# Optimization experiments

Hardware: AMD Instinct MI355X
Metric: run time of the kernel (lower is better)

Reference implementation:

```python
import jax, jax.numpy as jnp
import numpy as np

NB_HEAD = 16
SIZE_PER_HEAD = 64
D_MODEL = NB_HEAD * SIZE_PER_HEAD  # 1024
B, S = 4, 2048
NEG_BIG = 1e10


def setup_inputs() -> dict:
    key = jax.random.key(0)
    ks = jax.random.split(key, 9)
    glorot = lambda k, shape: jax.random.uniform(
        k, shape, jnp.float32, -1.0, 1.0) * np.sqrt(6.0 / (shape[0] + shape[1]))
    return {
        "Q_emb": jax.random.normal(ks[0], (B, S, D_MODEL), jnp.float32),
        "K_emb": jax.random.normal(ks[1], (B, S, D_MODEL), jnp.float32),
        "V_emb": jax.random.normal(ks[2], (B, S, D_MODEL), jnp.float32),
        "Q_ini": jax.random.randint(ks[3], (B, S), 0, 50),
        "K_ini": jax.random.randint(ks[4], (B, S), 0, 50),
        "WQ": glorot(ks[5], (D_MODEL, D_MODEL)),
        "WK": glorot(ks[6], (D_MODEL, D_MODEL)),
        "WV": glorot(ks[7], (D_MODEL, D_MODEL)),
        "WO": glorot(ks[8], (D_MODEL, D_MODEL)),
    }


def _proj(x, W):
    # [B,S,D] @ [D, H*dh] -> [B,H,S,dh]
    b, s, _ = x.shape
    y = jnp.einsum('bsd,de->bse', x, W)
    return y.reshape(b, s, NB_HEAD, SIZE_PER_HEAD).transpose(0, 2, 1, 3)


def reference(Q_emb, K_emb, V_emb, Q_ini, K_ini, WQ, WK, WV, WO):
    b, sq, _ = Q_emb.shape
    sk = K_emb.shape[1]
    q = _proj(Q_emb, WQ)
    k = _proj(K_emb, WK)
    v = _proj(V_emb, WV)
    scores = jnp.einsum('bhqd,bhkd->bhqk', q, k) / jnp.sqrt(
        jnp.asarray(SIZE_PER_HEAD, scores_dtype := q.dtype))
    # pad mask: 1 where key token id != 0, broadcast over queries
    pad = (K_ini != 0).astype(scores.dtype)[:, None, None, :]  # [B,1,1,Sk]
    # sub mask: cumsum of eye along rows == lower-triangular causal mask
    causal = jnp.tril(jnp.ones((sq, sk), scores.dtype))[None, None]  # [1,1,Sq,Sk]
    mask = jnp.minimum(pad, causal)
    scores = scores - (1.0 - mask) * NEG_BIG
    attn = jax.nn.softmax(scores, axis=-1)
    ctx = jnp.einsum('bhqk,bhkd->bhqd', attn, v)
    ctx = ctx.transpose(0, 2, 1, 3).reshape(b, sq, NB_HEAD * SIZE_PER_HEAD)
    return jnp.einsum('bsd,de->bse', ctx, WO)
```

## Files before the change

kernel.cpp:

```cpp
#include <hip/hip_runtime.h>

typedef __bf16 bf16_t;
typedef __bf16 bf16x8 __attribute__((ext_vector_type(8)));
typedef __bf16 bf16x4 __attribute__((ext_vector_type(4)));
typedef float  f32x4  __attribute__((ext_vector_type(4)));

#define S_LEN 2048
#define NH    16
#define DH    64
#define DM    1024
#define BATCH 4

static __device__ __forceinline__ f32x4 mfma16(bf16x8 a, bf16x8 b, f32x4 c) {
    return __builtin_amdgcn_mfma_f32_16x16x32_bf16(a, b, c, 0, 0, 0);
}

static __device__ __forceinline__ f32x4 fmax4(f32x4 a, f32x4 b) {
    f32x4 r;
    r[0] = fmaxf(a[0], b[0]); r[1] = fmaxf(a[1], b[1]);
    r[2] = fmaxf(a[2], b[2]); r[3] = fmaxf(a[3], b[3]);
    return r;
}

static __device__ __forceinline__ void gl_lds16(const bf16_t* g, bf16_t* l) {
    __builtin_amdgcn_global_load_lds(
        (const __attribute__((address_space(1))) unsigned int*)g,
        (__attribute__((address_space(3))) unsigned int*)l, 16, 0, 0);
}

__global__ __launch_bounds__(256) void cvt_bf16(const float* __restrict__ s,
                                                bf16_t* __restrict__ d, int n) {
    int i = (blockIdx.x * 256 + threadIdx.x) * 8;
    if (i >= n) return;
    const float4* q = (const float4*)(s + i);
    float4 a = q[0], b = q[1];
    bf16x8 r;
    r[0] = (bf16_t)a.x; r[1] = (bf16_t)a.y; r[2] = (bf16_t)a.z; r[3] = (bf16_t)a.w;
    r[4] = (bf16_t)b.x; r[5] = (bf16_t)b.y; r[6] = (bf16_t)b.z; r[7] = (bf16_t)b.w;
    *(bf16x8*)(d + i) = r;
}

__global__ __launch_bounds__(256) void wtrans(const float* __restrict__ W,
                                              bf16_t* __restrict__ Wt, float scale) {
    __shared__ bf16_t tile[32][33];
    int x = threadIdx.x, ty = threadIdx.y;
    int bx = blockIdx.x * 32, by = blockIdx.y * 32;
#pragma unroll
    for (int i = 0; i < 4; ++i) {
        int y = ty * 4 + i;
        tile[y][x] = (bf16_t)(W[(by + y) * DM + bx + x] * scale);
    }
    __syncthreads();
#pragma unroll
    for (int i = 0; i < 4; ++i) {
        int y = ty * 4 + i;
        Wt[(bx + y) * DM + by + x] = tile[x][y];
    }
}

__global__ __launch_bounds__(256) void btrans(const bf16_t* __restrict__ src,
                                              bf16_t* __restrict__ dst,
                                              int R, int C) {
    __shared__ bf16_t tile[32][33];
    int x = threadIdx.x, ty = threadIdx.y;
    int bx = blockIdx.x * 32, by = blockIdx.y * 32;
#pragma unroll
    for (int i = 0; i < 4; ++i) {
        int y = ty * 4 + i;
        tile[y][x] = src[(size_t)(by + y) * C + bx + x];
    }
    __syncthreads();
#pragma unroll
    for (int i = 0; i < 4; ++i) {
        int y = ty * 4 + i;
        dst[(size_t)(bx + y) * R + by + x] = tile[x][y];
    }
}

template <typename CT>
__global__ __launch_bounds__(256) void gemm_nt_128(const bf16_t* __restrict__ A,
                                                   const bf16_t* __restrict__ Bt,
                                                   CT* __restrict__ C,
                                                   int M, int N, int K, float alpha) {
    __shared__ __align__(16) bf16_t As[128 * 32];
    __shared__ __align__(16) bf16_t Bs[128 * 32];
    int tid = threadIdx.x, wave = tid >> 6, lane = tid & 63;
    int l15 = lane & 15, quad = lane >> 4;
    int wm = wave >> 1, wn = wave & 1;
    int bm = blockIdx.x * 128, bn = blockIdx.y * 128;
    int lrow = lane >> 2, lk = (lane & 3) << 3;

    f32x4 acc[4][4] = {};

    for (int k0 = 0; k0 < K; k0 += 32) {
#pragma unroll
        for (int c = 0; c < 2; ++c) {
            int r = wave * 32 + c * 16 + lrow;
            gl_lds16(A  + (size_t)(bm + r) * K + k0 + lk, As + (wave * 2 + c) * 512);
            gl_lds16(Bt + (size_t)(bn + r) * K + k0 + lk, Bs + (wave * 2 + c) * 512);
        }
        __syncthreads();

        bf16x8 af[4], bfr[4];
#pragma unroll
        for (int i = 0; i < 4; ++i)
            af[i] = *(const bf16x8*)(As + (wm * 64 + i * 16 + l15) * 32 + quad * 8);
#pragma unroll
        for (int j = 0; j < 4; ++j)
            bfr[j] = *(const bf16x8*)(Bs + (wn * 64 + j * 16 + l15) * 32 + quad * 8);
#pragma unroll
        for (int i = 0; i < 4; ++i)
#pragma unroll
            for (int j = 0; j < 4; ++j)
                acc[i][j] = mfma16(af[i], bfr[j], acc[i][j]);
        __syncthreads();
    }

#pragma unroll
    for (int i = 0; i < 4; ++i)
#pragma unroll
        for (int r = 0; r < 4; ++r) {
            int row = bm + wm * 64 + i * 16 + quad * 4 + r;
#pragma unroll
            for (int j = 0; j < 4; ++j)
                C[(size_t)row * N + bn + wn * 64 + j * 16 + l15] =
                    (CT)(acc[i][j][r] * alpha);
        }
}

__global__ __launch_bounds__(256) void vmean_kernel(const bf16_t* __restrict__ Vp,
                                                    float* __restrict__ Vm) {
    __shared__ float red[4][64];
    int z = blockIdx.y;
    int c = blockIdx.x * 64 + (threadIdx.x & 63);
    int rg = threadIdx.x >> 6;
    const bf16_t* p = Vp + (size_t)z * S_LEN * DM + (size_t)rg * (S_LEN / 4) * DM + c;
    float s = 0.f;
    for (int r = 0; r < S_LEN / 4; ++r) s += (float)p[(size_t)r * DM];
    red[rg][threadIdx.x & 63] = s;
    __syncthreads();
    if (threadIdx.x < 64) {
        float t = red[0][threadIdx.x] + red[1][threadIdx.x] +
                  red[2][threadIdx.x] + red[3][threadIdx.x];
        Vm[z * DM + blockIdx.x * 64 + threadIdx.x] = t * (1.0f / S_LEN);
    }
}

__global__ __launch_bounds__(256) void attn_kernel(const bf16_t* __restrict__ Qp,
                                                   const bf16_t* __restrict__ Kp,
                                                   const bf16_t* __restrict__ VT,
                                                   const int* __restrict__ Kini,
                                                   const float* __restrict__ Vmean,
                                                   bf16_t* __restrict__ ctx,
                                                   int ldv, int nqt) {
    __shared__ __align__(16) bf16_t Ks[64 * 72];
    __shared__ __align__(16) bf16_t VsT[64 * 72];
    __shared__ __align__(16) bf16_t Ps[4][16 * 72];
    __shared__ bf16_t padb[2048];

    int bid = blockIdx.x;
    int qt = nqt - 1 - (bid >> 6);
    int hz = bid & 63;
    int h = hz & 15, z = hz >> 4;
    int tid = threadIdx.x, wave = tid >> 6, lane = tid & 63;
    int l15 = lane & 15, quad = lane >> 4;
    int qbase = qt * 64 + wave * 16;
    size_t rowz = (size_t)z * S_LEN;
    int ntiles = qt + 1;
    int nkeys = ntiles * 64;

    for (int i = tid; i < nkeys; i += 256)
        padb[i] = (Kini[rowz + i] == 0) ? (bf16_t)(-1e10f) : (bf16_t)(0.0f);

    const bf16_t* qptr = Qp + (rowz + qbase + l15) * DM + h * DH + quad * 8;
    bf16x8 qa0 = *(const bf16x8*)qptr;
    bf16x8 qa1 = *(const bf16x8*)(qptr + 32);

    f32x4 o[4] = {};
    float m_ = -3.0e38f, l_ = 0.0f;
    int q = qbase + l15;

    int srow = tid >> 2, sch = (tid & 3) << 4;
    const bf16_t* kgb = Kp + (rowz + srow) * DM + h * DH + sch;
    const bf16_t* vgb = VT + (size_t)(h * DH + srow) * ldv + rowz + sch;

    bf16x8 kr0 = *(const bf16x8*)kgb,        kr1 = *(const bf16x8*)(kgb + 8);
    bf16x8 vr0 = *(const bf16x8*)vgb,        vr1 = *(const bf16x8*)(vgb + 8);

    for (int kt = 0; kt < ntiles; ++kt) {
        int kb = kt * 64;
        *(bf16x8*)(Ks  + srow * 72 + sch)     = kr0;
        *(bf16x8*)(Ks  + srow * 72 + sch + 8) = kr1;
        *(bf16x8*)(VsT + srow * 72 + sch)     = vr0;
        *(bf16x8*)(VsT + srow * 72 + sch + 8) = vr1;
        __syncthreads();

        int nkb = (kt + 1 < ntiles) ? kb + 64 : kb;
        const bf16_t* kg = kgb + (size_t)nkb * DM;
        const bf16_t* vg = vgb + nkb;
        kr0 = *(const bf16x8*)kg; kr1 = *(const bf16x8*)(kg + 8);
        vr0 = *(const bf16x8*)vg; vr1 = *(const bf16x8*)(vg + 8);

        f32x4 sv[4];
#pragma unroll
        for (int ks = 0; ks < 4; ++ks) {
            bf16x8 kf0 = *(const bf16x8*)(Ks + (ks * 16 + l15) * 72 + quad * 8);
            bf16x8 kf1 = *(const bf16x8*)(Ks + (ks * 16 + l15) * 72 + 32 + quad * 8);
            f32x4 s = {0.f, 0.f, 0.f, 0.f};
            s = mfma16(kf0, qa0, s);
            s = mfma16(kf1, qa1, s);
            bf16x4 pb = *(const bf16x4*)(padb + kb + ks * 16 + quad * 4);
#pragma unroll
            for (int r = 0; r < 4; ++r) s[r] += (float)pb[r];
            sv[ks] = s;
        }
        if (kt == ntiles - 1) {
#pragma unroll
            for (int ks = 0; ks < 4; ++ks)
#pragma unroll
                for (int r = 0; r < 4; ++r)
                    if (kb + ks * 16 + quad * 4 + r > q) sv[ks][r] = -1e10f;
        }

        f32x4 m4 = fmax4(fmax4(sv[0], sv[1]), fmax4(sv[2], sv[3]));
        float mx = fmaxf(fmaxf(m4[0], m4[1]), fmaxf(m4[2], m4[3]));
        mx = fmaxf(mx, __shfl_xor(mx, 16));
        mx = fmaxf(mx, __shfl_xor(mx, 32));

        if (__any(mx > m_ + 8.0f)) {
            float mn = fmaxf(m_, mx);
            float al = __expf(m_ - mn);
#pragma unroll
            for (int j = 0; j < 4; ++j) o[j] *= al;
            l_ *= al; m_ = mn;
        }

#pragma unroll
        for (int ks = 0; ks < 4; ++ks) {
            f32x4 s = sv[ks];
#pragma unroll
            for (int r = 0; r < 4; ++r) s[r] = __expf(s[r] - m_);
            sv[ks] = s;
        }
        f32x4 t4 = (sv[0] + sv[1]) + (sv[2] + sv[3]);
        float rs = (t4[0] + t4[1]) + (t4[2] + t4[3]);
        rs += __shfl_xor(rs, 16);
        rs += __shfl_xor(rs, 32);
        l_ += rs;
#pragma unroll
        for (int ks = 0; ks < 4; ++ks) {
            bf16x4 pk;
#pragma unroll
            for (int r = 0; r < 4; ++r) pk[r] = (bf16_t)sv[ks][r];
            *(bf16x4*)(Ps[wave] + l15 * 72 + ks * 16 + quad * 4) = pk;
        }

        bf16x8 pa0 = *(const bf16x8*)(Ps[wave] + l15 * 72 + quad * 8);
        bf16x8 pa1 = *(const bf16x8*)(Ps[wave] + l15 * 72 + 32 + quad * 8);
#pragma unroll
        for (int j = 0; j < 4; ++j) {
            bf16x8 vb0 = *(const bf16x8*)(VsT + (j * 16 + l15) * 72 + quad * 8);
            bf16x8 vb1 = *(const bf16x8*)(VsT + (j * 16 + l15) * 72 + 32 + quad * 8);
            o[j] = mfma16(vb0, pa0, o[j]);
            o[j] = mfma16(vb1, pa1, o[j]);
        }
        __syncthreads();
    }

    float inv = 1.0f / l_;
    bool dead = (m_ < -1e9f);
    if (__any(dead)) {
        const float* vm = Vmean + z * DM + h * DH;
#pragma unroll
        for (int j = 0; j < 4; ++j) {
            bf16x4 c;
#pragma unroll
            for (int r = 0; r < 4; ++r) {
                int dh = j * 16 + quad * 4 + r;
                float val = dead ? vm[dh] : o[j][r] * inv;
                c[r] = (bf16_t)val;
            }
            *(bf16x4*)(Ps[wave] + l15 * 72 + j * 16 + quad * 4) = c;
        }
    } else {
#pragma unroll
        for (int j = 0; j < 4; ++j) {
            bf16x4 c;
#pragma unroll
            for (int r = 0; r < 4; ++r) c[r] = (bf16_t)(o[j][r] * inv);
            *(bf16x4*)(Ps[wave] + l15 * 72 + j * 16 + quad * 4) = c;
        }
    }
    int rr = lane >> 2, cc = (lane & 3) * 16;
    bf16x8 t0 = *(const bf16x8*)(Ps[wave] + rr * 72 + cc);
    bf16x8 t1 = *(const bf16x8*)(Ps[wave] + rr * 72 + cc + 8);
    bf16_t* cp = ctx + (rowz + qbase + rr) * DM + h * DH + cc;
    *(bf16x8*)cp = t0;
    *(bf16x8*)(cp + 8) = t1;
}

extern "C" void kernel_launch(void* const* d_in, const int* in_sizes, int n_in,
                              void* d_out, int out_size, void* d_ws, size_t ws_size,
                              hipStream_t stream) {
    const float* Qe = (const float*)d_in[0];
    const float* Ke = (const float*)d_in[1];
    const float* Ve = (const float*)d_in[2];
    const int* Kini = (const int*)d_in[4];
    const float* WQ = (const float*)d_in[5];
    const float* WK = (const float*)d_in[6];
    const float* WV = (const float*)d_in[7];
    const float* WO = (const float*)d_in[8];
    float* out = (float*)d_out;

    const size_t EMB = (size_t)BATCH * S_LEN * DM;
    const size_t SB  = (size_t)S_LEN * DM;
    const size_t WSZ = (size_t)DM * DM;
    const size_t need_full = (6 * EMB + 4 * WSZ) * sizeof(bf16_t)
                           + (size_t)BATCH * DM * sizeof(float);

    dim3 tb32(32, 8), tg32(32, 32);

    if (ws_size >= need_full) {
        bf16_t* Qb  = (bf16_t*)d_ws;
        bf16_t* Kb  = Qb + EMB;
        bf16_t* Vb  = Kb + EMB;
        bf16_t* WQt = Vb + EMB;
        bf16_t* WKt = WQt + WSZ;
        bf16_t* WVt = WKt + WSZ;
        bf16_t* WOt = WVt + WSZ;
        bf16_t* Qp  = WOt + WSZ;
        bf16_t* Kp  = Qp + EMB;
        bf16_t* Vp  = Kp + EMB;
        float*  Vm  = (float*)(Vp + EMB);
        bf16_t* Cx  = Qp;
        bf16_t* VT  = Vb;

        int cg = (int)(EMB / (8 * 256));
        cvt_bf16<<<cg, 256, 0, stream>>>(Qe, Qb, (int)EMB);
        cvt_bf16<<<cg, 256, 0, stream>>>(Ke, Kb, (int)EMB);
        cvt_bf16<<<cg, 256, 0, stream>>>(Ve, Vb, (int)EMB);
        wtrans<<<tg32, tb32, 0, stream>>>(WQ, WQt, 0.125f);
        wtrans<<<tg32, tb32, 0, stream>>>(WK, WKt, 1.0f);
        wtrans<<<tg32, tb32, 0, stream>>>(WV, WVt, 1.0f);
        wtrans<<<tg32, tb32, 0, stream>>>(WO, WOt, 1.0f);

        dim3 gg(8192 / 128, DM / 128);
        gemm_nt_128<bf16_t><<<gg, 256, 0, stream>>>(Qb, WQt, Qp, 8192, DM, DM, 1.0f);
        gemm_nt_128<bf16_t><<<gg, 256, 0, stream>>>(Kb, WKt, Kp, 8192, DM, DM, 1.0f);
        gemm_nt_128<bf16_t><<<gg, 256, 0, stream>>>(Vb, WVt, Vp, 8192, DM, DM, 1.0f);

        btrans<<<dim3(DM / 32, 8192 / 32), tb32, 0, stream>>>(Vp, VT, 8192, DM);
        vmean_kernel<<<dim3(DM / 64, BATCH), 256, 0, stream>>>(Vp, Vm);
        attn_kernel<<<dim3((S_LEN / 64) * NH * BATCH), 256, 0, stream>>>(
            Qp, Kp, VT, Kini, Vm, Cx, 8192, S_LEN / 64);

        gemm_nt_128<float><<<gg, 256, 0, stream>>>(Cx, WOt, out, 8192, DM, DM, 1.0f);
    } else {
        bf16_t* Qb  = (bf16_t*)d_ws;
        bf16_t* Kb  = Qb + SB;
        bf16_t* Vb  = Kb + SB;
        bf16_t* WQt = Vb + SB;
        bf16_t* WKt = WQt + WSZ;
        bf16_t* WVt = WKt + WSZ;
        bf16_t* WOt = WVt + WSZ;
        bf16_t* Qp  = WOt + WSZ;
        bf16_t* Kp  = Qp + SB;
        bf16_t* Vp  = Kp + SB;
        float*  Vm  = (float*)(Vp + SB);
        bf16_t* Cx  = Qp;
        bf16_t* VT  = Vb;

        wtrans<<<tg32, tb32, 0, stream>>>(WQ, WQt, 0.125f);
        wtrans<<<tg32, tb32, 0, stream>>>(WK, WKt, 1.0f);
        wtrans<<<tg32, tb32, 0, stream>>>(WV, WVt, 1.0f);
        wtrans<<<tg32, tb32, 0, stream>>>(WO, WOt, 1.0f);

        int cg = (int)(SB / (8 * 256));
        dim3 gg(2048 / 128, DM / 128);
        for (int b = 0; b < BATCH; ++b) {
            const size_t off = (size_t)b * SB;
            cvt_bf16<<<cg, 256, 0, stream>>>(Qe + off, Qb, (int)SB);
            cvt_bf16<<<cg, 256, 0, stream>>>(Ke + off, Kb, (int)SB);
            cvt_bf16<<<cg, 256, 0, stream>>>(Ve + off, Vb, (int)SB);
            gemm_nt_128<bf16_t><<<gg, 256, 0, stream>>>(Qb, WQt, Qp, 2048, DM, DM, 1.0f);
            gemm_nt_128<bf16_t><<<gg, 256, 0, stream>>>(Kb, WKt, Kp, 2048, DM, DM, 1.0f);
            gemm_nt_128<bf16_t><<<gg, 256, 0, stream>>>(Vb, WVt, Vp, 2048, DM, DM, 1.0f);
            btrans<<<dim3(DM / 32, 2048 / 32), tb32, 0, stream>>>(Vp, VT, 2048, DM);
            vmean_kernel<<<dim3(DM / 64, 1), 256, 0, stream>>>(Vp, Vm);
            attn_kernel<<<dim3((S_LEN / 64) * NH), 256, 0, stream>>>(
                Qp, Kp, VT, Kini + (size_t)b * S_LEN, Vm, Cx, 2048, S_LEN / 64);
            gemm_nt_128<float><<<gg, 256, 0, stream>>>(Cx, WOt, out + off, 2048, DM, DM, 1.0f);
        }
    }
}
```

Baseline: 383.2 us.

## Batch QKV GEMMs in one launch, deepen K-step, use exp2 softmax

Merges the three Q/K/V projection GEMMs into a single launch that uses blockIdx.z, relying on the buffers being laid out contiguously. The GEMM now loads a 64-wide K slice per barrier pair instead of 32, which halves the number of syncs. The softmax switches to exp2f with log2e folded into the Q weight scale, and the rescale threshold is raised to match the log2 domain. This trades more LDS per block for fewer launches and fewer barriers.

Measured after the change: 363.9 us. 1.05x faster.

```diff
diff --git a/kernel.cpp b/kernel.cpp
--- a/kernel.cpp
+++ b/kernel.cpp
@@ -10,6 +10,7 @@
 #define DH    64
 #define DM    1024
 #define BATCH 4
+#define LOG2E 1.44269504088896f
 
 static __device__ __forceinline__ f32x4 mfma16(bf16x8 a, bf16x8 b, f32x4 c) {
     return __builtin_amdgcn_mfma_f32_16x16x32_bf16(a, b, c, 0, 0, 0);
@@ -78,41 +79,53 @@
 }
 
 template <typename CT>
-__global__ __launch_bounds__(256) void gemm_nt_128(const bf16_t* __restrict__ A,
-                                                   const bf16_t* __restrict__ Bt,
-                                                   CT* __restrict__ C,
-                                                   int M, int N, int K, float alpha) {
-    __shared__ __align__(16) bf16_t As[128 * 32];
-    __shared__ __align__(16) bf16_t Bs[128 * 32];
+__global__ __launch_bounds__(256) void gemm_nt_64(const bf16_t* __restrict__ A,
+                                                  const bf16_t* __restrict__ Bt,
+                                                  CT* __restrict__ C,
+                                                  int M, int N, int K, float alpha,
+                                                  size_t zsA, size_t zsB, size_t zsC) {
+    __shared__ __align__(16) bf16_t As[2 * 128 * 32];
+    __shared__ __align__(16) bf16_t Bs[2 * 128 * 32];
+    A  += (size_t)blockIdx.z * zsA;
+    Bt += (size_t)blockIdx.z * zsB;
+    C  += (size_t)blockIdx.z * zsC;
     int tid = threadIdx.x, wave = tid >> 6, lane = tid & 63;
     int l15 = lane & 15, quad = lane >> 4;
     int wm = wave >> 1, wn = wave & 1;
     int bm = blockIdx.x * 128, bn = blockIdx.y * 128;
-    int lrow = lane >> 2, lk = (lane & 3) << 3;
+    int srow = lane >> 2, skx = (lane & 3) << 3;
 
     f32x4 acc[4][4] = {};
 
-    for (int k0 = 0; k0 < K; k0 += 32) {
-#pragma unroll
-        for (int c = 0; c < 2; ++c) {
-            int r = wave * 32 + c * 16 + lrow;
-            gl_lds16(A  + (size_t)(bm + r) * K + k0 + lk, As + (wave * 2 + c) * 512);
-            gl_lds16(Bt + (size_t)(bn + r) * K + k0 + lk, Bs + (wave * 2 + c) * 512);
+    for (int k0 = 0; k0 < K; k0 += 64) {
+#pragma unroll
+        for (int c = 0; c < 4; ++c) {
+            int t = wave * 4 + c;
+            int kk = t & 1, rb = (t >> 1) * 16;
+            gl_lds16(A  + (size_t)(bm + rb + srow) * K + k0 + kk * 32 + skx,
+                     As + kk * 4096 + rb * 32);
+            gl_lds16(Bt + (size_t)(bn + rb + srow) * K + k0 + kk * 32 + skx,
+                     Bs + kk * 4096 + rb * 32);
         }
         __syncthreads();
 
-        bf16x8 af[4], bfr[4];
-#pragma unroll
-        for (int i = 0; i < 4; ++i)
-            af[i] = *(const bf16x8*)(As + (wm * 64 + i * 16 + l15) * 32 + quad * 8);
-#pragma unroll
-        for (int j = 0; j < 4; ++j)
-            bfr[j] = *(const bf16x8*)(Bs + (wn * 64 + j * 16 + l15) * 32 + quad * 8);
-#pragma unroll
-        for (int i = 0; i < 4; ++i)
+#pragma unroll
+        for (int kk = 0; kk < 2; ++kk) {
+            bf16x8 af[4], bfr[4];
+#pragma unroll
+            for (int i = 0; i < 4; ++i)
+                af[i] = *(const bf16x8*)(As + kk * 4096 +
+                                         (wm * 64 + i * 16 + l15) * 32 + quad * 8);
 #pragma unroll
             for (int j = 0; j < 4; ++j)
-                acc[i][j] = mfma16(af[i], bfr[j], acc[i][j]);
+                bfr[j] = *(const bf16x8*)(Bs + kk * 4096 +
+                                          (wn * 64 + j * 16 + l15) * 32 + quad * 8);
+#pragma unroll
+            for (int i = 0; i < 4; ++i)
+#pragma unroll
+                for (int j = 0; j < 4; ++j)
+                    acc[i][j] = mfma16(af[i], bfr[j], acc[i][j]);
+        }
         __syncthreads();
     }
 
@@ -170,7 +183,7 @@
     int nkeys = ntiles * 64;
 
     for (int i = tid; i < nkeys; i += 256)
-        padb[i] = (Kini[rowz + i] == 0) ? (bf16_t)(-1e10f) : (bf16_t)(0.0f);
+        padb[i] = (Kini[rowz + i] == 0) ? (bf16_t)(-1.44269504e10f) : (bf16_t)(0.0f);
 
     const bf16_t* qptr = Qp + (rowz + qbase + l15) * DM + h * DH + quad * 8;
     bf16x8 qa0 = *(const bf16x8*)qptr;
@@ -219,7 +232,7 @@
             for (int ks = 0; ks < 4; ++ks)
 #pragma unroll
                 for (int r = 0; r < 4; ++r)
-                    if (kb + ks * 16 + quad * 4 + r > q) sv[ks][r] = -1e10f;
+                    if (kb + ks * 16 + quad * 4 + r > q) sv[ks][r] = -1.44269504e10f;
         }
 
         f32x4 m4 = fmax4(fmax4(sv[0], sv[1]), fmax4(sv[2], sv[3]));
@@ -227,9 +240,9 @@
         mx = fmaxf(mx, __shfl_xor(mx, 16));
         mx = fmaxf(mx, __shfl_xor(mx, 32));
 
-        if (__any(mx > m_ + 8.0f)) {
+        if (__any(mx > m_ + 12.0f)) {
             float mn = fmaxf(m_, mx);
-            float al = __expf(m_ - mn);
+            float al = exp2f(m_ - mn);
 #pragma unroll
             for (int j = 0; j < 4; ++j) o[j] *= al;
             l_ *= al; m_ = mn;
@@ -239,7 +252,7 @@
         for (int ks = 0; ks < 4; ++ks) {
             f32x4 s = sv[ks];
 #pragma unroll
-            for (int r = 0; r < 4; ++r) s[r] = __expf(s[r] - m_);
+            for (int r = 0; r < 4; ++r) s[r] = exp2f(s[r] - m_);
             sv[ks] = s;
         }
         f32x4 t4 = (sv[0] + sv[1]) + (sv[2] + sv[3]);
@@ -319,6 +332,7 @@
                            + (size_t)BATCH * DM * sizeof(float);
 
     dim3 tb32(32, 8), tg32(32, 32);
+    const float qscale = 0.125f * LOG2E;
 
     if (ws_size >= need_full) {
         bf16_t* Qb  = (bf16_t*)d_ws;
@@ -339,22 +353,21 @@
         cvt_bf16<<<cg, 256, 0, stream>>>(Qe, Qb, (int)EMB);
         cvt_bf16<<<cg, 256, 0, stream>>>(Ke, Kb, (int)EMB);
         cvt_bf16<<<cg, 256, 0, stream>>>(Ve, Vb, (int)EMB);
-        wtrans<<<tg32, tb32, 0, stream>>>(WQ, WQt, 0.125f);
+        wtrans<<<tg32, tb32, 0, stream>>>(WQ, WQt, qscale);
         wtrans<<<tg32, tb32, 0, stream>>>(WK, WKt, 1.0f);
         wtrans<<<tg32, tb32, 0, stream>>>(WV, WVt, 1.0f);
         wtrans<<<tg32, tb32, 0, stream>>>(WO, WOt, 1.0f);
 
-        dim3 gg(8192 / 128, DM / 128);
-        gemm_nt_128<bf16_t><<<gg, 256, 0, stream>>>(Qb, WQt, Qp, 8192, DM, DM, 1.0f);
-        gemm_nt_128<bf16_t><<<gg, 256, 0, stream>>>(Kb, WKt, Kp, 8192, DM, DM, 1.0f);
-        gemm_nt_128<bf16_t><<<gg, 256, 0, stream>>>(Vb, WVt, Vp, 8192, DM, DM, 1.0f);
+        gemm_nt_64<bf16_t><<<dim3(8192 / 128, DM / 128, 3), 256, 0, stream>>>(
+            Qb, WQt, Qp, 8192, DM, DM, 1.0f, EMB, WSZ, EMB);
 
         btrans<<<dim3(DM / 32, 8192 / 32), tb32, 0, stream>>>(Vp, VT, 8192, DM);
         vmean_kernel<<<dim3(DM / 64, BATCH), 256, 0, stream>>>(Vp, Vm);
         attn_kernel<<<dim3((S_LEN / 64) * NH * BATCH), 256, 0, stream>>>(
             Qp, Kp, VT, Kini, Vm, Cx, 8192, S_LEN / 64);
 
-        gemm_nt_128<float><<<gg, 256, 0, stream>>>(Cx, WOt, out, 8192, DM, DM, 1.0f);
+        gemm_nt_64<float><<<dim3(8192 / 128, DM / 128, 1), 256, 0, stream>>>(
+            Cx, WOt, out, 8192, DM, DM, 1.0f, 0, 0, 0);
     } else {
         bf16_t* Qb  = (bf16_t*)d_ws;
         bf16_t* Kb  = Qb + SB;
@@ -370,26 +383,25 @@
         bf16_t* Cx  = Qp;
         bf16_t* VT  = Vb;
 
-        wtrans<<<tg32, tb32, 0, stream>>>(WQ, WQt, 0.125f);
+        wtrans<<<tg32, tb32, 0, stream>>>(WQ, WQt, qscale);
         wtrans<<<tg32, tb32, 0, stream>>>(WK, WKt, 1.0f);
         wtrans<<<tg32, tb32, 0, stream>>>(WV, WVt, 1.0f);
         wtrans<<<tg32, tb32, 0, stream>>>(WO, WOt, 1.0f);
 
         int cg = (int)(SB / (8 * 256));
-        dim3 gg(2048 / 128, DM / 128);
         for (int b = 0; b < BATCH; ++b) {
             const size_t off = (size_t)b * SB;
             cvt_bf16<<<cg, 256, 0, stream>>>(Qe + off, Qb, (int)SB);
             cvt_bf16<<<cg, 256, 0, stream>>>(Ke + off, Kb, (int)SB);
             cvt_bf16<<<cg, 256, 0, stream>>>(Ve + off, Vb, (int)SB);
-            gemm_nt_128<bf16_t><<<gg, 256, 0, stream>>>(Qb, WQt, Qp, 2048, DM, DM, 1.0f);
-            gemm_nt_128<bf16_t><<<gg, 256, 0, stream>>>(Kb, WKt, Kp, 2048, DM, DM, 1.0f);
-            gemm_nt_128<bf16_t><<<gg, 256, 0, stream>>>(Vb, WVt, Vp, 2048, DM, DM, 1.0f);
+            gemm_nt_64<bf16_t><<<dim3(2048 / 128, DM / 128, 3), 256, 0, stream>>>(
+                Qb, WQt, Qp, 2048, DM, DM, 1.0f, SB, WSZ, SB);
             btrans<<<dim3(DM / 32, 2048 / 32), tb32, 0, stream>>>(Vp, VT, 2048, DM);
             vmean_kernel<<<dim3(DM / 64, 1), 256, 0, stream>>>(Vp, Vm);
             attn_kernel<<<dim3((S_LEN / 64) * NH), 256, 0, stream>>>(
                 Qp, Kp, VT, Kini + (size_t)b * S_LEN, Vm, Cx, 2048, S_LEN / 64);
-            gemm_nt_128<float><<<gg, 256, 0, stream>>>(Cx, WOt, out + off, 2048, DM, DM, 1.0f);
-        }
-    }
-}
+            gemm_nt_64<float><<<dim3(2048 / 128, DM / 128, 1), 256, 0, stream>>>(
+                Cx, WOt, out + off, 2048, DM, DM, 1.0f, 0, 0, 0);
+        }
+    }
+}
```
